# Kernel tuning notes

Hardware: AMD Instinct MI355X
Metric: run time of the kernel (lower is better)

## Reference

```python
import jax, jax.numpy as jnp
import numpy as np

MARGIN = 0.1
NUM_BINS = 1600  # FastAP histogram bins over squared-distance range [0, 4]


def _fastap_rewards(x, labels):
    """Per-query FastAP (Cakir et al.) with soft (triangular) histogram binning.
    x: [n, d] L2-normalized embeddings; labels: [n] int. Returns [n] rewards.
    Uses the fact that a triangular pulse of width delta spreads each distance
    over exactly two adjacent bins -> scatter-add instead of an [n,n,L] tensor."""
    n = x.shape[0]
    L = NUM_BINS + 1
    delta = 4.0 / NUM_BINS
    dist2 = jnp.clip(2.0 - 2.0 * (x @ x.T), 0.0, 4.0)  # [n, n]
    same = labels[:, None] == labels[None, :]
    eye = jnp.eye(n, dtype=bool)
    i_pos = same & ~eye
    i_neg = ~same

    t = dist2 / delta
    idx0 = jnp.clip(jnp.floor(t).astype(jnp.int32), 0, L - 1)
    idx1 = jnp.clip(idx0 + 1, 0, L - 1)
    frac = t - jnp.floor(t)
    rows = jnp.broadcast_to(jnp.arange(n)[:, None], (n, n))

    def hist(mask):
        m = mask.astype(x.dtype)
        h = jnp.zeros((n, L), x.dtype)
        h = h.at[rows, idx0].add((1.0 - frac) * m)
        h = h.at[rows, idx1].add(frac * m)
        return h

    h_pos = hist(i_pos)
    h_neg = hist(i_neg)
    H_pos = jnp.cumsum(h_pos, axis=1)
    H_all = jnp.cumsum(h_pos + h_neg, axis=1)
    n_pos = jnp.sum(i_pos, axis=1).astype(x.dtype)
    safe = H_all > 0
    ap = jnp.sum(jnp.where(safe, h_pos * H_pos / jnp.where(safe, H_all, 1.0), 0.0), axis=1)
    return jnp.where(n_pos > 0, ap / jnp.maximum(n_pos, 1.0), 0.0)


def _per_row_loss(inputs_col, targets_col, inputs_row, targets_row):
    """Vectorized form of compute_loss_list. Sorting in the original only serves
    to extract max pos / max neg similarity, so per-row maxima + masked sums
    reproduce the exact same math."""
    n = inputs_col.shape[0]
    sim = inputs_col @ inputs_row.T  # [n, m]
    pos = targets_col[:, None] == targets_row[None, :]
    neg = ~pos  # computed BEFORE removing the diagonal, as in the original
    eye = jnp.eye(n, dtype=bool)
    pos = pos.at[:, :n].set(pos[:, :n] & ~eye)

    has_pos = jnp.any(pos, axis=1)
    neg_max = jnp.max(jnp.where(neg, sim, -jnp.inf), axis=1)  # neg_pair_[-1]
    pos_max = jnp.max(jnp.where(pos, sim, -jnp.inf), axis=1)  # pos_pair_[-1]

    pos_sel = pos & (sim < (neg_max + MARGIN)[:, None])
    pos_loss = jnp.sum(jnp.where(pos_sel, 1.0 - sim, 0.0), axis=1)

    thr = jnp.maximum(0.6, pos_max) - MARGIN
    neg_sel = neg & (sim > thr[:, None])
    neg_loss = jnp.sum(jnp.where(neg_sel, sim, 0.0), axis=1)

    return jnp.where(has_pos, pos_loss + neg_loss, 0.0), n


def setup_inputs() -> dict:
    key = jax.random.key(0)
    k1, k2, k3, k4, k5 = jax.random.split(key, 5)
    n, m, d, ncls = 4096, 4096, 128, 512

    def unit(k, shape):
        v = jax.random.normal(k, shape, dtype=jnp.float32)
        return v / jnp.linalg.norm(v, axis=-1, keepdims=True)

    return {
        "inputs_col": unit(k1, (n, d)),
        "targets_col": jax.random.randint(k2, (n,), 0, ncls),
        "inputs_row": unit(k3, (m, d)),
        "targets_row": jax.random.randint(k4, (m,), 0, ncls),
        "reward_labels": jax.random.randint(k5, (n,), 0, ncls),
    }


def reference(inputs_col, targets_col, inputs_row, targets_row, reward_labels):
    loss_i, n = _per_row_loss(inputs_col, targets_col, inputs_row, targets_row)
    # torch.tensor(rewards) detaches rewards from the graph -> stop_gradient
    rewards = jax.lax.stop_gradient(_fastap_rewards(inputs_col, reward_labels))
    return jnp.sum(loss_i * (1.0 - rewards)) / n
```

## Files before the change

kernel.cpp:

```cpp
#include <hip/hip_runtime.h>


#define N_ROWS 4096
#define DIM 128
#define TILE 128
#define L_BINS 1601

typedef __bf16 bf16x8 __attribute__((ext_vector_type(8)));
typedef float f32x4 __attribute__((ext_vector_type(4)));

__device__ __forceinline__ unsigned short f32_to_bf16(float f) {
    unsigned int u = __float_as_uint(f);
    u = (u + 0x7FFFu + ((u >> 16) & 1u)) >> 16;
    return (unsigned short)u;
}
__device__ __forceinline__ unsigned int pack2(float x, float y) {
    return (unsigned int)f32_to_bf16(x) | ((unsigned int)f32_to_bf16(y) << 16);
}
__device__ __forceinline__ float bf16_lo(unsigned int u) { return __uint_as_float(u << 16); }
__device__ __forceinline__ float bf16_hi(unsigned int u) { return __uint_as_float(u & 0xFFFF0000u); }

__device__ __forceinline__ void unpack8(uint4 pk, float* s) {
    s[0] = bf16_lo(pk.x); s[1] = bf16_hi(pk.x);
    s[2] = bf16_lo(pk.y); s[3] = bf16_hi(pk.y);
    s[4] = bf16_lo(pk.z); s[5] = bf16_hi(pk.z);
    s[6] = bf16_lo(pk.w); s[7] = bf16_hi(pk.w);
}

__global__ __launch_bounds__(256) void gemm_kernel(
    const float* __restrict__ incol, const float* __restrict__ inrow,
    unsigned short* __restrict__ simbuf, unsigned short* __restrict__ grambuf) {
    __shared__ __align__(16) unsigned short As[TILE * DIM];
    __shared__ __align__(16) unsigned short Bs[TILE * DIM];
    int t = threadIdx.x;
    int w = t >> 6, lane = t & 63;
    int tm = blockIdx.y, tn = blockIdx.x;
    const float* ga = incol + (size_t)tm * TILE * DIM;
    const float* gb = (blockIdx.z ? incol : inrow) + (size_t)tn * TILE * DIM;
    unsigned short* C = blockIdx.z ? grambuf : simbuf;

#pragma unroll
    for (int it = 0; it < 8; ++it) {
        int fo = it * 2048 + t * 8;
        float4 a0 = *(const float4*)(ga + fo);
        float4 a1 = *(const float4*)(ga + fo + 4);
        float4 b0 = *(const float4*)(gb + fo);
        float4 b1 = *(const float4*)(gb + fo + 4);
        uint4 pa, pb;
        pa.x = pack2(a0.x, a0.y); pa.y = pack2(a0.z, a0.w);
        pa.z = pack2(a1.x, a1.y); pa.w = pack2(a1.z, a1.w);
        pb.x = pack2(b0.x, b0.y); pb.y = pack2(b0.z, b0.w);
        pb.z = pack2(b1.x, b1.y); pb.w = pack2(b1.z, b1.w);
        *(uint4*)((char*)As + it * 4096 + t * 16) = pa;
        *(uint4*)((char*)Bs + it * 4096 + t * 16) = pb;
    }
    __syncthreads();

    int wm = (w & 1) * 64;
    int wn = (w >> 1) * 64;
    int quad = lane >> 4;
    int l15 = lane & 15;
    f32x4 acc[4][4] = {};
#pragma unroll
    for (int kk = 0; kk < 4; ++kk) {
        int kb = kk * 32 + quad * 8;
        bf16x8 af[4], bfr[4];
#pragma unroll
        for (int mi = 0; mi < 4; ++mi)
            af[mi] = *(const bf16x8*)&As[(wm + mi * 16 + l15) * DIM + kb];
#pragma unroll
        for (int ni = 0; ni < 4; ++ni)
            bfr[ni] = *(const bf16x8*)&Bs[(wn + ni * 16 + l15) * DIM + kb];
#pragma unroll
        for (int mi = 0; mi < 4; ++mi)
#pragma unroll
            for (int ni = 0; ni < 4; ++ni)
                acc[mi][ni] = __builtin_amdgcn_mfma_f32_16x16x32_bf16(af[mi], bfr[ni], acc[mi][ni], 0, 0, 0);
    }
#pragma unroll
    for (int mi = 0; mi < 4; ++mi) {
        int row0 = tm * TILE + wm + mi * 16 + quad * 4;
#pragma unroll
        for (int ni = 0; ni < 4; ++ni) {
            int col = tn * TILE + wn + ni * 16 + l15;
#pragma unroll
            for (int r = 0; r < 4; ++r)
                C[(size_t)(row0 + r) * N_ROWS + col] = f32_to_bf16(acc[mi][ni][r]);
        }
    }
}

__global__ __launch_bounds__(256) void tail_kernel(
    const unsigned short* __restrict__ simbuf, const unsigned short* __restrict__ grambuf,
    const int* __restrict__ tcol, const int* __restrict__ trow, const int* __restrict__ rlab,
    float* __restrict__ lossv, float* __restrict__ rewardv) {
    __shared__ unsigned int h_pos[L_BINS];
    __shared__ unsigned int h_all[L_BINS];
    __shared__ unsigned long long wsumA[4];
    __shared__ float apwA[4];
    __shared__ int npwA[4];
    int b = blockIdx.x;
    int t = threadIdx.x;
    int w = t >> 6, lane = t & 63;

    if (b < 1024) {
        int i = b * 4 + w;
        int myt = tcol[i];
        const uint4* simv = (const uint4*)(simbuf + (size_t)i * N_ROWS);
        const int4* labv = (const int4*)trow;
        float pmax = -3e38f, nmax = -3e38f;
#pragma unroll
        for (int v = 0; v < 8; ++v) {
            int vi = v * 64 + lane;
            uint4 pk = simv[vi];
            int4 l0 = labv[2 * vi];
            int4 l1 = labv[2 * vi + 1];
            int j0 = vi * 8;
            float s[8];
            unpack8(pk, s);
            int lab[8] = {l0.x, l0.y, l0.z, l0.w, l1.x, l1.y, l1.z, l1.w};
#pragma unroll
            for (int k = 0; k < 8; ++k) {
                int j = j0 + k;
                bool same = (lab[k] == myt);
                if (same && (j != i)) pmax = fmaxf(pmax, s[k]);
                if (!same) nmax = fmaxf(nmax, s[k]);
            }
        }
#pragma unroll
        for (int off = 32; off > 0; off >>= 1) {
            pmax = fmaxf(pmax, __shfl_xor(pmax, off));
            nmax = fmaxf(nmax, __shfl_xor(nmax, off));
        }
        float thr_n = nmax + 0.1f;
        float thr_p = fmaxf(0.6f, pmax) - 0.1f;
        float pl = 0.f, nl = 0.f;
#pragma unroll
        for (int v = 0; v < 8; ++v) {
            int vi = v * 64 + lane;
            uint4 pk = simv[vi];
            int4 l0 = labv[2 * vi];
            int4 l1 = labv[2 * vi + 1];
            int j0 = vi * 8;
            float s[8];
            unpack8(pk, s);
            int lab[8] = {l0.x, l0.y, l0.z, l0.w, l1.x, l1.y, l1.z, l1.w};
#pragma unroll
            for (int k = 0; k < 8; ++k) {
                int j = j0 + k;
                bool same = (lab[k] == myt);
                pl += (same && (j != i) && s[k] < thr_n) ? 1.f - s[k] : 0.f;
                nl += (!same && s[k] > thr_p) ? s[k] : 0.f;
            }
        }
        float tot = pl + nl;
#pragma unroll
        for (int off = 32; off > 0; off >>= 1) tot += __shfl_xor(tot, off);
        if (lane == 0) lossv[i] = (pmax > -1e30f) ? tot : 0.f;
    } else {
        int i = b - 1024;
        for (int bb = t; bb < L_BINS; bb += 256) { h_pos[bb] = 0u; h_all[bb] = 0u; }
        __syncthreads();
        int li = rlab[i];
        int npos = 0;
        const uint4* gv = (const uint4*)(grambuf + (size_t)i * N_ROWS);
        const int4* labv = (const int4*)rlab;
        for (int v = t; v < (N_ROWS >> 3); v += 256) {
            uint4 pk = gv[v];
            int4 l0 = labv[2 * v];
            int4 l1 = labv[2 * v + 1];
            int j0 = v << 3;
            float s[8];
            unpack8(pk, s);
            int lab[8] = {l0.x, l0.y, l0.z, l0.w, l1.x, l1.y, l1.z, l1.w};
#pragma unroll
            for (int k = 0; k < 8; ++k) {
                int j = j0 + k;
                if (j == i) continue;
                float d2 = fminf(fmaxf(2.f - 2.f * s[k], 0.f), 4.f);
                float tt = d2 * 400.0f;
                float fl = floorf(tt);
                int i0 = (int)fl;
                if (i0 > L_BINS - 1) i0 = L_BINS - 1;
                int i1 = i0 + 1;
                if (i1 > L_BINS - 1) i1 = L_BINS - 1;
                unsigned int w1 = (unsigned int)((tt - fl) * 65536.0f);
                unsigned int w0 = 65536u - w1;
                atomicAdd(&h_all[i0], w0);
                atomicAdd(&h_all[i1], w1);
                if (lab[k] == li) {
                    atomicAdd(&h_pos[i0], w0);
                    atomicAdd(&h_pos[i1], w1);
                    npos++;
                }
            }
        }
        __syncthreads();

        const int CH = 7;
        int base = t * CH;
        unsigned long long lc[CH];
        unsigned long long run = 0ull;
#pragma unroll
        for (int k = 0; k < CH; ++k) {
            int idx = base + k;
            unsigned long long h = 0ull;
            if (idx < L_BINS)
                h = (unsigned long long)h_all[idx] | ((unsigned long long)h_pos[idx] << 32);
            run += h;
            lc[k] = run;
        }
        unsigned long long tsum = run;
        unsigned long long sc = tsum;
#pragma unroll
        for (int off = 1; off < 64; off <<= 1) {
            unsigned long long v2 = __shfl_up(sc, off);
            if (lane >= off) sc += v2;
        }
        if (lane == 63) wsumA[w] = sc;
        __syncthreads();
        unsigned long long woff = 0ull;
        for (int ww = 0; ww < w; ++ww) woff += wsumA[ww];
        unsigned long long throff = woff + sc - tsum;

        float ap = 0.f;
#pragma unroll
        for (int k = 0; k < CH; ++k) {
            int idx = base + k;
            if (idx < L_BINS) {
                unsigned int hp = h_pos[idx];
                if (hp) {
                    unsigned long long cum = lc[k] + throff;
                    ap += (float)hp * (float)(unsigned int)(cum >> 32) / (float)(unsigned int)cum;
                }
            }
        }
#pragma unroll
        for (int off = 32; off > 0; off >>= 1) {
            ap += __shfl_xor(ap, off);
            npos += __shfl_xor(npos, off);
        }
        if (lane == 0) { apwA[w] = ap; npwA[w] = npos; }
        __syncthreads();
        if (t == 0) {
            float A = apwA[0] + apwA[1] + apwA[2] + apwA[3];
            int np = npwA[0] + npwA[1] + npwA[2] + npwA[3];
            rewardv[i] = (np > 0) ? A * (1.0f / 65536.0f) / (float)np : 0.f;
        }
    }
}

__global__ __launch_bounds__(256) void final_kernel(const float* __restrict__ lossv,
                                                    const float* __restrict__ rewardv,
                                                    float* __restrict__ out) {
    __shared__ float r[4];
    int t = threadIdx.x;
    int w = t >> 6, lane = t & 63;
    float s = 0.f;
    for (int j = t; j < N_ROWS; j += 256) s += lossv[j] * (1.f - rewardv[j]);
#pragma unroll
    for (int off = 32; off > 0; off >>= 1) s += __shfl_xor(s, off);
    if (lane == 0) r[w] = s;
    __syncthreads();
    if (t == 0) out[0] = (r[0] + r[1] + r[2] + r[3]) / (float)N_ROWS;
}

extern "C" void kernel_launch(void* const* d_in, const int* in_sizes, int n_in,
                              void* d_out, int out_size, void* d_ws, size_t ws_size,
                              hipStream_t stream) {
    const float* inputs_col = (const float*)d_in[0];
    const int* targets_col = (const int*)d_in[1];
    const float* inputs_row = (const float*)d_in[2];
    const int* targets_row = (const int*)d_in[3];
    const int* reward_labels = (const int*)d_in[4];
    float* out = (float*)d_out;

    char* ws = (char*)d_ws;
    const size_t MB = 1048576;
    unsigned short* simbuf = (unsigned short*)ws;
    unsigned short* grambuf = (unsigned short*)(ws + 32 * MB);
    float* lossv = (float*)(ws + 64 * MB);
    float* rewardv = (float*)(ws + 64 * MB + 16384);

    dim3 ggrid(N_ROWS / TILE, N_ROWS / TILE, 2);
    gemm_kernel<<<ggrid, 256, 0, stream>>>(inputs_col, inputs_row, simbuf, grambuf);

    tail_kernel<<<1024 + N_ROWS, 256, 0, stream>>>(simbuf, grambuf,
                                                   targets_col, targets_row, reward_labels,
                                                   lossv, rewardv);

    final_kernel<<<1, 256, 0, stream>>>(lossv, rewardv, out);
}
```

Baseline: 143.1 us.

## Fuse per-row pos/neg max reduction into GEMM epilogue via atomicMax

```diff
diff --git a/kernel.cpp b/kernel.cpp
--- a/kernel.cpp
+++ b/kernel.cpp
@@ -27,17 +27,34 @@
     s[6] = bf16_lo(pk.w); s[7] = bf16_hi(pk.w);
 }
 
+__device__ __forceinline__ unsigned int enc_f(float f) {
+    unsigned int u = __float_as_uint(f);
+    return (u & 0x80000000u) ? ~u : (u | 0x80000000u);
+}
+__device__ __forceinline__ float dec_f(unsigned int k) {
+    return (k & 0x80000000u) ? __uint_as_float(k & 0x7FFFFFFFu) : __uint_as_float(~k);
+}
+
 __global__ __launch_bounds__(256) void gemm_kernel(
     const float* __restrict__ incol, const float* __restrict__ inrow,
-    unsigned short* __restrict__ simbuf, unsigned short* __restrict__ grambuf) {
+    const int* __restrict__ tcol, const int* __restrict__ trow,
+    unsigned short* __restrict__ simbuf, unsigned short* __restrict__ grambuf,
+    unsigned int* __restrict__ maxpos, unsigned int* __restrict__ maxneg) {
     __shared__ __align__(16) unsigned short As[TILE * DIM];
     __shared__ __align__(16) unsigned short Bs[TILE * DIM];
+    __shared__ int rlabs[TILE];
+    __shared__ int clabs[TILE];
     int t = threadIdx.x;
     int w = t >> 6, lane = t & 63;
     int tm = blockIdx.y, tn = blockIdx.x;
     const float* ga = incol + (size_t)tm * TILE * DIM;
     const float* gb = (blockIdx.z ? incol : inrow) + (size_t)tn * TILE * DIM;
     unsigned short* C = blockIdx.z ? grambuf : simbuf;
+
+    if (blockIdx.z == 0) {
+        if (t < TILE) rlabs[t] = tcol[tm * TILE + t];
+        else clabs[t - TILE] = trow[tn * TILE + (t - TILE)];
+    }
 
 #pragma unroll
     for (int it = 0; it < 8; ++it) {
@@ -77,6 +94,7 @@
             for (int ni = 0; ni < 4; ++ni)
                 acc[mi][ni] = __builtin_amdgcn_mfma_f32_16x16x32_bf16(af[mi], bfr[ni], acc[mi][ni], 0, 0, 0);
     }
+
 #pragma unroll
     for (int mi = 0; mi < 4; ++mi) {
         int row0 = tm * TILE + wm + mi * 16 + quad * 4;
@@ -86,6 +104,42 @@
 #pragma unroll
             for (int r = 0; r < 4; ++r)
                 C[(size_t)(row0 + r) * N_ROWS + col] = f32_to_bf16(acc[mi][ni][r]);
+        }
+    }
+
+    if (blockIdx.z == 0) {
+        int clv[4], gcol[4];
+#pragma unroll
+        for (int ni = 0; ni < 4; ++ni) {
+            clv[ni] = clabs[wn + ni * 16 + l15];
+            gcol[ni] = tn * TILE + wn + ni * 16 + l15;
+        }
+#pragma unroll
+        for (int mi = 0; mi < 4; ++mi) {
+#pragma unroll
+            for (int r = 0; r < 4; ++r) {
+                int lrow = wm + mi * 16 + quad * 4 + r;
+                int grow = tm * TILE + lrow;
+                int rl = rlabs[lrow];
+                float pm = -3e38f, nm = -3e38f;
+#pragma unroll
+                for (int ni = 0; ni < 4; ++ni) {
+                    float s = bf16_lo((unsigned int)f32_to_bf16(acc[mi][ni][r]));
+                    bool same = (clv[ni] == rl);
+                    bool diag = (gcol[ni] == grow);
+                    if (same && !diag) pm = fmaxf(pm, s);
+                    if (!same) nm = fmaxf(nm, s);
+                }
+#pragma unroll
+                for (int off = 1; off < 16; off <<= 1) {
+                    pm = fmaxf(pm, __shfl_xor(pm, off));
+                    nm = fmaxf(nm, __shfl_xor(nm, off));
+                }
+                if (l15 == 0) {
+                    if (pm > -2e38f) atomicMax(&maxpos[grow], enc_f(pm));
+                    if (nm > -2e38f) atomicMax(&maxneg[grow], enc_f(nm));
+                }
+            }
         }
     }
 }
@@ -93,6 +147,7 @@
 __global__ __launch_bounds__(256) void tail_kernel(
     const unsigned short* __restrict__ simbuf, const unsigned short* __restrict__ grambuf,
     const int* __restrict__ tcol, const int* __restrict__ trow, const int* __restrict__ rlab,
+    const unsigned int* __restrict__ maxpos, const unsigned int* __restrict__ maxneg,
     float* __restrict__ lossv, float* __restrict__ rewardv) {
     __shared__ unsigned int h_pos[L_BINS];
     __shared__ unsigned int h_all[L_BINS];
@@ -103,62 +158,8 @@
     int t = threadIdx.x;
     int w = t >> 6, lane = t & 63;
 
-    if (b < 1024) {
-        int i = b * 4 + w;
-        int myt = tcol[i];
-        const uint4* simv = (const uint4*)(simbuf + (size_t)i * N_ROWS);
-        const int4* labv = (const int4*)trow;
-        float pmax = -3e38f, nmax = -3e38f;
-#pragma unroll
-        for (int v = 0; v < 8; ++v) {
-            int vi = v * 64 + lane;
-            uint4 pk = simv[vi];
-            int4 l0 = labv[2 * vi];
-            int4 l1 = labv[2 * vi + 1];
-            int j0 = vi * 8;
-            float s[8];
-            unpack8(pk, s);
-            int lab[8] = {l0.x, l0.y, l0.z, l0.w, l1.x, l1.y, l1.z, l1.w};
-#pragma unroll
-            for (int k = 0; k < 8; ++k) {
-                int j = j0 + k;
-                bool same = (lab[k] == myt);
-                if (same && (j != i)) pmax = fmaxf(pmax, s[k]);
-                if (!same) nmax = fmaxf(nmax, s[k]);
-            }
-        }
-#pragma unroll
-        for (int off = 32; off > 0; off >>= 1) {
-            pmax = fmaxf(pmax, __shfl_xor(pmax, off));
-            nmax = fmaxf(nmax, __shfl_xor(nmax, off));
-        }
-        float thr_n = nmax + 0.1f;
-        float thr_p = fmaxf(0.6f, pmax) - 0.1f;
-        float pl = 0.f, nl = 0.f;
-#pragma unroll
-        for (int v = 0; v < 8; ++v) {
-            int vi = v * 64 + lane;
-            uint4 pk = simv[vi];
-            int4 l0 = labv[2 * vi];
-            int4 l1 = labv[2 * vi + 1];
-            int j0 = vi * 8;
-            float s[8];
-            unpack8(pk, s);
-            int lab[8] = {l0.x, l0.y, l0.z, l0.w, l1.x, l1.y, l1.z, l1.w};
-#pragma unroll
-            for (int k = 0; k < 8; ++k) {
-                int j = j0 + k;
-                bool same = (lab[k] == myt);
-                pl += (same && (j != i) && s[k] < thr_n) ? 1.f - s[k] : 0.f;
-                nl += (!same && s[k] > thr_p) ? s[k] : 0.f;
-            }
-        }
-        float tot = pl + nl;
-#pragma unroll
-        for (int off = 32; off > 0; off >>= 1) tot += __shfl_xor(tot, off);
-        if (lane == 0) lossv[i] = (pmax > -1e30f) ? tot : 0.f;
-    } else {
-        int i = b - 1024;
+    if (b < N_ROWS) {
+        int i = b;
         for (int bb = t; bb < L_BINS; bb += 256) { h_pos[bb] = 0u; h_all[bb] = 0u; }
         __syncthreads();
         int li = rlab[i];
@@ -247,17 +248,55 @@
             int np = npwA[0] + npwA[1] + npwA[2] + npwA[3];
             rewardv[i] = (np > 0) ? A * (1.0f / 65536.0f) / (float)np : 0.f;
         }
-    }
-}
-
-__global__ __launch_bounds__(256) void final_kernel(const float* __restrict__ lossv,
-                                                    const float* __restrict__ rewardv,
+    } else {
+        int i = (b - N_ROWS) * 4 + w;
+        int myt = tcol[i];
+        unsigned int pke = maxpos[i];
+        bool has_pos = (pke != 0u);
+        float pmax = dec_f(pke);
+        float nmax = dec_f(maxneg[i]);
+        float thr_n = nmax + 0.1f;
+        float thr_p = fmaxf(0.6f, pmax) - 0.1f;
+        const uint4* simv = (const uint4*)(simbuf + (size_t)i * N_ROWS);
+        const int4* labv = (const int4*)trow;
+        float pl = 0.f, nl = 0.f;
+#pragma unroll
+        for (int v = 0; v < 8; ++v) {
+            int vi = v * 64 + lane;
+            uint4 pk = simv[vi];
+            int4 l0 = labv[2 * vi];
+            int4 l1 = labv[2 * vi + 1];
+            int j0 = vi * 8;
+            float s[8];
+            unpack8(pk, s);
+            int lab[8] = {l0.x, l0.y, l0.z, l0.w, l1.x, l1.y, l1.z, l1.w};
+#pragma unroll
+            for (int k = 0; k < 8; ++k) {
+                int j = j0 + k;
+                bool same = (lab[k] == myt);
+                pl += (same && (j != i) && s[k] < thr_n) ? 1.f - s[k] : 0.f;
+                nl += (!same && s[k] > thr_p) ? s[k] : 0.f;
+            }
+        }
+        float tot = pl + nl;
+#pragma unroll
+        for (int off = 32; off > 0; off >>= 1) tot += __shfl_xor(tot, off);
+        if (lane == 0) lossv[i] = has_pos ? tot : 0.f;
+    }
+}
+
+__global__ __launch_bounds__(256) void final_kernel(const float4* __restrict__ lossv,
+                                                    const float4* __restrict__ rewardv,
                                                     float* __restrict__ out) {
     __shared__ float r[4];
     int t = threadIdx.x;
     int w = t >> 6, lane = t & 63;
     float s = 0.f;
-    for (int j = t; j < N_ROWS; j += 256) s += lossv[j] * (1.f - rewardv[j]);
+    for (int j = t; j < N_ROWS / 4; j += 256) {
+        float4 lv = lossv[j];
+        float4 rv = rewardv[j];
+        s += lv.x * (1.f - rv.x) + lv.y * (1.f - rv.y) + lv.z * (1.f - rv.z) + lv.w * (1.f - rv.w);
+    }
 #pragma unroll
     for (int off = 32; off > 0; off >>= 1) s += __shfl_xor(s, off);
     if (lane == 0) r[w] = s;
@@ -281,13 +320,19 @@
     unsigned short* grambuf = (unsigned short*)(ws + 32 * MB);
     float* lossv = (float*)(ws + 64 * MB);
     float* rewardv = (float*)(ws + 64 * MB + 16384);
+    unsigned int* maxpos = (unsigned int*)(ws + 64 * MB + 32768);
+    unsigned int* maxneg = (unsigned int*)(ws + 64 * MB + 49152);
+
+    hipMemsetAsync(maxpos, 0, 2 * 16384, stream);
 
     dim3 ggrid(N_ROWS / TILE, N_ROWS / TILE, 2);
-    gemm_kernel<<<ggrid, 256, 0, stream>>>(inputs_col, inputs_row, simbuf, grambuf);
-
-    tail_kernel<<<1024 + N_ROWS, 256, 0, stream>>>(simbuf, grambuf,
+    gemm_kernel<<<ggrid, 256, 0, stream>>>(inputs_col, inputs_row,
+                                           targets_col, targets_row,
+                                           simbuf, grambuf, maxpos, maxneg);
+
+    tail_kernel<<<N_ROWS + 1024, 256, 0, stream>>>(simbuf, grambuf,
                                                    targets_col, targets_row, reward_labels,
-                                                   lossv, rewardv);
-
-    final_kernel<<<1, 256, 0, stream>>>(lossv, rewardv, out);
-}
+                                                   maxpos, maxneg, lossv, rewardv);
+
+    final_kernel<<<1, 256, 0, stream>>>((const float4*)lossv, (const float4*)rewardv, out);
+}
```

New measurement: 156.5 us. 9.3% more time.
